# Performance work log

Measured on AMD Instinct MI355X. Metric: run time of the kernel, lower is better.

## Reference

```python
import jax, jax.numpy as jnp
import numpy as np

PAD, BOS, EOS, UNK = 0, 1, 2, 3
B, S, V, D, L = 256, 512, 50000, 256, 128

def setup_inputs() -> dict:
    key = jax.random.key(0)
    ks = jax.random.split(key, 12)
    vocab_tensor = jax.random.randint(ks[0], (B, S), 4, V)
    parent_idx = jax.random.randint(ks[1], (B, S), 0, S)
    pbond = jax.random.randint(ks[2], (B, S), 0, 4)
    bond = jax.random.randint(ks[3], (B, S), 0, 4)
    patom = jax.random.randint(ks[4], (B, S), 0, 16)
    atom = jax.random.randint(ks[5], (B, S), 0, 16)
    btype = jax.random.randint(ks[6], (B, S), 0, 4)
    order_tensor = jnp.stack([parent_idx, pbond, bond, patom, atom, btype], axis=-1)
    lengths = jax.random.randint(ks[7], (B,), 1, S + 1)
    mask_tensor = jnp.arange(S)[None, :] < lengths[:, None]  # ragged prefix masks
    eps = jax.random.normal(ks[8], (B, L), dtype=jnp.float32)
    sc = 1.0 / np.sqrt(D)
    emb = jax.random.normal(ks[9], (V, D), dtype=jnp.float32) * sc
    Wm = jax.random.normal(ks[10], (D, L), dtype=jnp.float32) * sc
    Wv = jax.random.normal(ks[11], (D, L), dtype=jnp.float32) * sc
    Wlin = jax.random.normal(jax.random.fold_in(key, 20), (L, D), dtype=jnp.float32) / np.sqrt(L)
    Wout = jax.random.normal(jax.random.fold_in(key, 21), (D, D), dtype=jnp.float32) * sc
    return {
        'vocab_tensor': vocab_tensor, 'order_tensor': order_tensor, 'mask_tensor': mask_tensor,
        'eps': eps, 'emb': emb, 'Wm': Wm, 'bm': jnp.zeros((L,), jnp.float32),
        'Wv': Wv, 'bv': jnp.zeros((L,), jnp.float32), 'Wlin': Wlin,
        'blin': jnp.zeros((D,), jnp.float32), 'Wout': Wout, 'bout': jnp.zeros((D,), jnp.float32),
    }

def _forward(vocab_tensor, order_tensor, mask_tensor, eps, emb, Wm, bm, Wv, bv, Wlin, blin, Wout, bout):
    # --- mask bond-pos columns (torch.where assignments, vectorized) ---
    # (columns 1 and 2 set to -1 where masked; kept implicitly via vt/pad handling)
    # --- calc_chem_z path: masked vocab, parent gather, edge one-hot ---
    vt = jnp.where(mask_tensor, vocab_tensor, PAD)                      # [B,S]
    vocab_emb = emb[vt]                                                 # [B,S,D]
    oi = order_tensor[..., 0]
    oi = jnp.where(oi == -1, BOS, oi)
    parent = jnp.where(mask_tensor, jnp.take_along_axis(vt, oi, axis=1), PAD)
    parent = parent.at[:, 0].set(BOS)
    parent_emb = emb[parent]                                            # [B,S,D]
    idx = jnp.clip(order_tensor[..., 5] - 1, -1, None)
    edge_type = jnp.where((idx >= 0)[..., None],
                          jax.nn.one_hot(jnp.clip(idx, 0), 3, dtype=jnp.float32), 0.0)  # [B,S,3]
    # pooling stand-in for (undefined) StructureEncoder -> [B,D]
    m = mask_tensor[..., None].astype(jnp.float32)
    enc = ((vocab_emb + parent_emb) * m).sum(1) / jnp.maximum(m.sum(1), 1.0)
    enc = enc * (1.0 + 0.0 * edge_type.sum())  # keep edge_type in graph
    # --- LatentSampler ---
    mean = enc @ Wm + bm
    log_var = enc @ Wv + bv
    z = mean + eps * jnp.exp(0.5 * log_var)
    memory = z @ Wlin + blin                                            # [B,D]
    # --- vectorized bos/eos/pad sequence assembly (the hot loop in torch) ---
    inp = jnp.concatenate([jnp.full((B, 1), BOS, vocab_tensor.dtype), vocab_tensor], axis=1)  # [B,S+1]
    mask_ex = jnp.concatenate([jnp.ones((B, 1), bool), mask_tensor], axis=1)
    tgt = jnp.roll(inp, -1, axis=1)
    first_false = jnp.argmax(~mask_ex, axis=1)                          # first eos position
    has_false = jnp.any(~mask_ex, axis=1)
    pos = jnp.arange(S + 1)[None, :]
    tgt = jnp.where(has_false[:, None] & (pos == first_false[:, None] - 1), EOS, tgt)
    kill = has_false[:, None] & (pos >= first_false[:, None])
    tgt = jnp.where(kill, PAD, tgt)
    inp = jnp.where(kill, PAD, inp)
    # edge_index assembly (faithful, consumed by decoder in original)
    padneg = jnp.full((B, 1), -1, order_tensor.dtype)
    edge_index = jnp.concatenate([padneg, jnp.where(mask_tensor, order_tensor[..., 0], -2) + 1], axis=1)
    # --- embedding lookups + decoder stand-in + output head ---
    node_embed = emb[inp]                                               # [B,S+1,D]
    dec = node_embed + memory[:, None, :]
    dec = dec + 0.0 * edge_index[..., None].astype(jnp.float32)         # keep edge_index in graph
    word_emb = dec @ Wout + bout
    tgt_emb = emb[tgt]
    valid = (tgt != PAD)
    sq = (word_emb - tgt_emb) ** 2 * valid[..., None]
    token_loss = sq.sum() / jnp.maximum(valid.sum() * D, 1).astype(jnp.float32)
    kl = -0.5 * jnp.sum(1.0 + log_var - mean ** 2 - jnp.exp(log_var)) / B
    return token_loss, kl

def reference(vocab_tensor, order_tensor, mask_tensor, eps, emb, Wm, bm, Wv, bv, Wlin, blin, Wout, bout):
    return _forward(vocab_tensor, order_tensor, mask_tensor, eps, emb, Wm, bm, Wv, bv, Wlin, blin, Wout, bout)
```

## Files before the change

### kernel.cpp

```cpp
#include <hip/hip_runtime.h>

#define B_ 256
#define S_ 512
#define V_ 50000
#define D_ 256
#define L_ 128
#define NGB 512
#define NENC 256
#define NCH (V_ / 16)
#define NSPLIT 8
#define K2B (B_ * NSPLIT)

typedef __attribute__((ext_vector_type(8))) short short8;
typedef __attribute__((ext_vector_type(4))) float floatx4;

#define OFF_SQP 16
#define OFF_KL  (OFF_SQP + K2B)
#define OFF_CNT (OFF_KL + 256)
#define OFF_Q   (OFF_CNT + 256)
#define OFF_P   (OFF_Q + B_ * D_)

__device__ __forceinline__ unsigned short f2bf(float x) {
    unsigned u = __float_as_uint(x);
    u += 0x7FFFu + ((u >> 16) & 1u);
    return (unsigned short)(u >> 16);
}
__device__ __forceinline__ float bf2f(unsigned short u) {
    return __uint_as_float(((unsigned)u) << 16);
}

__global__ __launch_bounds__(256, 2) void fused1(
    const int* __restrict__ vocab, const int* __restrict__ order,
    const int* __restrict__ mask, const float* __restrict__ emb,
    const float* __restrict__ eps, const float* __restrict__ Wm,
    const float* __restrict__ bm, const float* __restrict__ Wv,
    const float* __restrict__ bv, const float* __restrict__ Wlin,
    const float* __restrict__ blin, const float* __restrict__ Wout,
    const float* __restrict__ bout, float* __restrict__ ws) {
    __shared__ __align__(16) char smem[11904];
    const int tid = threadIdx.x;

    if (blockIdx.x < NGB) {
        unsigned short* __restrict__ P = (unsigned short*)(ws + OFF_P);
        const int lane = tid & 63, wv = tid >> 6;
        const int lo = lane & 15, hi = lane >> 4;
        short8 bfr[4][8];
#pragma unroll
        for (int nt = 0; nt < 4; ++nt)
#pragma unroll
            for (int kk = 0; kk < 8; ++kk) {
                const float* wp = Wout + (size_t)(hi * 8 + kk * 32) * D_ +
                                  wv * 64 + nt * 16 + lo;
                short8 w;
#pragma unroll
                for (int e = 0; e < 8; ++e) w[e] = (short)f2bf(wp[(size_t)e * D_]);
                bfr[nt][kk] = w;
            }
        int ch = blockIdx.x;
        float4 R[4];
        {
            const float4* src = (const float4*)emb + (size_t)ch * 1024;
#pragma unroll
            for (int i = 0; i < 4; ++i) R[i] = src[i * 256 + tid];
        }
        for (; ch < NCH; ch += NGB) {
#pragma unroll
            for (int i = 0; i < 4; ++i) {
                const int e = (i * 256 + tid) * 4;
                const int row = e >> 8, colb = (e & 255) * 2;
                const int byt = (row * 512 + colb) ^ ((row & 7) << 4);
                ushort4 h;
                h.x = f2bf(R[i].x); h.y = f2bf(R[i].y);
                h.z = f2bf(R[i].z); h.w = f2bf(R[i].w);
                *(ushort4*)(smem + byt) = h;
            }
            __syncthreads();
            const int chn = ch + NGB;
            float4 Rn[4] = {R[0], R[1], R[2], R[3]};
            if (chn < NCH) {
                const float4* src = (const float4*)emb + (size_t)chn * 1024;
#pragma unroll
                for (int i = 0; i < 4; ++i) Rn[i] = src[i * 256 + tid];
            }
            floatx4 acc[4];
#pragma unroll
            for (int nt = 0; nt < 4; ++nt) acc[nt] = (floatx4){0.f, 0.f, 0.f, 0.f};
#pragma unroll
            for (int kk = 0; kk < 8; ++kk) {
                const int byt = (lo * 512 + hi * 16 + kk * 64) ^ ((lo & 7) << 4);
                short8 a = *(const short8*)(smem + byt);
#pragma unroll
                for (int nt = 0; nt < 4; ++nt)
                    acc[nt] = __builtin_amdgcn_mfma_f32_16x16x32_bf16(
                        a, bfr[nt][kk], acc[nt], 0, 0, 0);
            }
#pragma unroll
            for (int r = 0; r < 4; ++r) {
                unsigned short* prow =
                    P + (size_t)(ch * 16 + hi * 4 + r) * D_ + wv * 64 + lo;
#pragma unroll
                for (int nt = 0; nt < 4; ++nt) prow[nt * 16] = f2bf(acc[nt][r]);
            }
            __syncthreads();
#pragma unroll
            for (int i = 0; i < 4; ++i) R[i] = Rn[i];
        }
        return;
    }
    int* s_id1 = (int*)smem;
    int* s_id2 = s_id1 + S_;
    float4* s_part = (float4*)(smem + 4096);
    float* s_enc = (float*)(smem + 7168);
    float* s_mean = (float*)(smem + 8192);
    float* s_lv = (float*)(smem + 8704);
    float* s_z = (float*)(smem + 9216);
    float* s_mem = (float*)(smem + 9728);
    float* s_red = (float*)(smem + 10752);
    int* s_cntp = (int*)(smem + 11776);
    const int b = blockIdx.x - NGB;
    if (tid == 0) *s_cntp = 0;
    __syncthreads();
    for (int j = tid; j < S_; j += 256) {
        const int mk = mask[b * S_ + j];
        int id1 = 0, id2 = 0;
        if (mk) {
            id1 = vocab[b * S_ + j];
            if (j == 0) {
                id2 = 1;
            } else {
                int oi = order[(size_t)(b * S_ + j) * 6];
                if (oi == -1) oi = 1;
                id2 = mask[b * S_ + oi] ? vocab[b * S_ + oi] : 0;
            }
        }
        s_id1[j] = id1;
        s_id2[j] = id2;
        unsigned long long bal = __ballot(mk != 0);
        if ((tid & 63) == 0) atomicAdd(s_cntp, __popcll(bal));
    }
    __syncthreads();
    const int cnt = *s_cntp;
    const int jg = tid >> 6, d4 = tid & 63;
    const float4* eb4 = (const float4*)emb;
    float4 a = {0.f, 0.f, 0.f, 0.f};
#pragma unroll 4
    for (int j = jg; j < cnt; j += 4) {
        float4 x = eb4[(size_t)s_id1[j] * 64 + d4];
        float4 y = eb4[(size_t)s_id2[j] * 64 + d4];
        a.x += x.x + y.x; a.y += x.y + y.y;
        a.z += x.z + y.z; a.w += x.w + y.w;
    }
    if (jg) s_part[(jg - 1) * 64 + d4] = a;
    __syncthreads();
    if (jg == 0) {
#pragma unroll
        for (int g = 0; g < 3; ++g) {
            float4 p = s_part[g * 64 + d4];
            a.x += p.x; a.y += p.y; a.z += p.z; a.w += p.w;
        }
        const float inv = 1.f / fmaxf((float)cnt, 1.f);
        a.x *= inv; a.y *= inv; a.z *= inv; a.w *= inv;
        ((float4*)s_enc)[d4] = a;
    }
    __syncthreads();
    {
        const int l = tid & (L_ - 1);
        const float* W = (tid < L_) ? Wm : Wv;
        const float* bb = (tid < L_) ? bm : bv;
        float dot = bb[l];
        for (int d = 0; d < D_; ++d) dot = fmaf(s_enc[d], W[d * L_ + l], dot);
        if (tid < L_) s_mean[l] = dot; else s_lv[l] = dot;
    }
    __syncthreads();
    float klp = 0.f;
    if (tid < L_) {
        float mn = s_mean[tid], lv = s_lv[tid];
        s_z[tid] = mn + eps[b * L_ + tid] * expf(0.5f * lv);
        klp = 1.f + lv - mn * mn - expf(lv);
    }
    s_red[tid] = klp;
    __syncthreads();
    for (int s = 128; s > 0; s >>= 1) {
        if (tid < s) s_red[tid] += s_red[tid + s];
        __syncthreads();
    }
    if (tid == 0) {
        ws[OFF_KL + b] = s_red[0];
        ((int*)ws)[OFF_CNT + b] = cnt;
    }
    {
        float mem = blin[tid];
        for (int l2 = 0; l2 < L_; ++l2) mem = fmaf(s_z[l2], Wlin[l2 * D_ + tid], mem);
        s_mem[tid] = mem;
    }
    __syncthreads();
    {
        float qv = bout[tid];
        for (int k = 0; k < D_; ++k) qv = fmaf(s_mem[k], Wout[k * D_ + tid], qv);
        ws[OFF_Q + b * D_ + tid] = qv;
    }
}

__global__ __launch_bounds__(256) void scan2(const int* __restrict__ vocab,
                                             const float* __restrict__ emb,
                                             float* __restrict__ ws) {
    __shared__ int s_sid[80];
    __shared__ float s_wred[4];
    const int tid = threadIdx.x;
    const int b = blockIdx.x >> 3, part = blockIdx.x & 7;
    const unsigned short* __restrict__ P = (const unsigned short*)(ws + OFF_P);
    const int cnt = ((const int*)ws)[OFF_CNT + b];
    const int npos = cnt + 1;
    const int per = (npos + NSPLIT - 1) / NSPLIT;
    const int j0 = part * per;
    const int jend = min(j0 + per, npos);
    const int lo_s = (j0 > 0) ? j0 - 1 : 0;
    const int nstage = min(jend, cnt) - lo_s;
    if (tid < nstage) s_sid[tid] = vocab[b * S_ + lo_s + tid];
    __syncthreads();
    const int jgq = tid >> 6, lane = tid & 63, c = lane * 4;
    const float4 q4 = *(const float4*)(ws + OFF_Q + b * D_ + c);
    float acc = 0.f;
    for (int jj = j0 + jgq * 4; jj < jend; jj += 16) {
        int inp[4], tgt[4];
        float wgt[4];
#pragma unroll
        for (int u = 0; u < 4; ++u) {
            const int j = jj + u;
            const bool v = (j < jend);
            const int jc = v ? j : jj;
            inp[u] = (jc == 0) ? 1 : s_sid[jc - 1 - lo_s];
            tgt[u] = (jc < cnt) ? s_sid[jc - lo_s] : ((cnt < S_) ? 2 : 1);
            wgt[u] = v ? 1.f : 0.f;
        }
        ushort4 pv[4];
        float4 tv[4];
#pragma unroll
        for (int u = 0; u < 4; ++u) {
            pv[u] = *(const ushort4*)(P + (size_t)inp[u] * D_ + c);
            tv[u] = *(const float4*)(emb + (size_t)tgt[u] * D_ + c);
        }
#pragma unroll
        for (int u = 0; u < 4; ++u) {
            float d0 = bf2f(pv[u].x) + q4.x - tv[u].x;
            float d1 = bf2f(pv[u].y) + q4.y - tv[u].y;
            float d2 = bf2f(pv[u].z) + q4.z - tv[u].z;
            float d3 = bf2f(pv[u].w) + q4.w - tv[u].w;
            float s = fmaf(d0, d0, fmaf(d1, d1, fmaf(d2, d2, d3 * d3)));
            acc = fmaf(wgt[u], s, acc);
        }
    }
#pragma unroll
    for (int off = 32; off; off >>= 1) acc += __shfl_down(acc, off, 64);
    if (lane == 0) s_wred[jgq] = acc;
    __syncthreads();
    if (tid == 0)
        ws[OFF_SQP + blockIdx.x] = s_wred[0] + s_wred[1] + s_wred[2] + s_wred[3];
}

__global__ __launch_bounds__(256) void finalize3(const float* __restrict__ ws,
                                                 float* __restrict__ out) {
    __shared__ float s_red[256];
    const int tid = threadIdx.x;
    float sq = 0.f;
#pragma unroll
    for (int i = 0; i < NSPLIT; ++i) sq += ws[OFF_SQP + i * 256 + tid];
    s_red[tid] = sq;
    __syncthreads();
    for (int s = 128; s > 0; s >>= 1) {
        if (tid < s) s_red[tid] += s_red[tid + s];
        __syncthreads();
    }
    const float sq_tot = s_red[0];
    __syncthreads();
    s_red[tid] = ws[OFF_KL + tid];
    __syncthreads();
    for (int s = 128; s > 0; s >>= 1) {
        if (tid < s) s_red[tid] += s_red[tid + s];
        __syncthreads();
    }
    const float kl_tot = s_red[0];
    __syncthreads();
    s_red[tid] = (float)(((const int*)ws)[OFF_CNT + tid] + 1);
    __syncthreads();
    for (int s = 128; s > 0; s >>= 1) {
        if (tid < s) s_red[tid] += s_red[tid + s];
        __syncthreads();
    }
    if (tid == 0) {
        float denom = s_red[0] * (float)D_;
        if (denom < 1.f) denom = 1.f;
        out[0] = sq_tot / denom;
        out[1] = -0.5f * kl_tot / (float)B_;
    }
}

extern "C" void kernel_launch(void* const* d_in, const int* in_sizes, int n_in,
                              void* d_out, int out_size, void* d_ws, size_t ws_size,
                              hipStream_t stream) {
    const int* vocab = (const int*)d_in[0];
    const int* order = (const int*)d_in[1];
    const int* mask  = (const int*)d_in[2];
    const float* eps  = (const float*)d_in[3];
    const float* emb  = (const float*)d_in[4];
    const float* Wm   = (const float*)d_in[5];
    const float* bm   = (const float*)d_in[6];
    const float* Wv   = (const float*)d_in[7];
    const float* bv   = (const float*)d_in[8];
    const float* Wlin = (const float*)d_in[9];
    const float* blin = (const float*)d_in[10];
    const float* Wout = (const float*)d_in[11];
    const float* bout = (const float*)d_in[12];

    float* ws = (float*)d_ws;
    fused1<<<NGB + NENC, 256, 0, stream>>>(vocab, order, mask, emb, eps, Wm, bm,
                                           Wv, bv, Wlin, blin, Wout, bout, ws);
    scan2<<<K2B, 256, 0, stream>>>(vocab, emb, ws);
    finalize3<<<1, 256, 0, stream>>>(ws, (float*)d_out);
}
```

Measured before the change: 172.0 us.

## Emit bf16 embedding copy and stage projected rows through LDS for coalesced stores

The fused projection kernel now writes a bf16 copy of each embedding chunk (already converted in shared memory) to a workspace buffer. Its projected output rows are staged through shared memory so they can be written with wide coalesced stores instead of scattered 2-byte stores. The scan kernel then gathers target embeddings as bf16 rather than fp32, halving the bytes of its random row reads. The cost is an extra bf16 table write per pass, a larger shared-memory footprint, and lower precision in the loss target term.

New measurement: 172.2 us. About the same (+0.1%).

```diff
diff --git a/kernel.cpp b/kernel.cpp
--- a/kernel.cpp
+++ b/kernel.cpp
@@ -19,6 +19,7 @@
 #define OFF_CNT (OFF_KL + 256)
 #define OFF_Q   (OFF_CNT + 256)
 #define OFF_P   (OFF_Q + B_ * D_)
+#define OFF_EB  (OFF_P + V_ * D_ / 2)
 
 __device__ __forceinline__ unsigned short f2bf(float x) {
     unsigned u = __float_as_uint(x);
@@ -37,11 +38,12 @@
     const float* __restrict__ bv, const float* __restrict__ Wlin,
     const float* __restrict__ blin, const float* __restrict__ Wout,
     const float* __restrict__ bout, float* __restrict__ ws) {
-    __shared__ __align__(16) char smem[11904];
+    __shared__ __align__(16) char smem[16384];
     const int tid = threadIdx.x;
 
     if (blockIdx.x < NGB) {
         unsigned short* __restrict__ P = (unsigned short*)(ws + OFF_P);
+        unsigned short* __restrict__ EB = (unsigned short*)(ws + OFF_EB);
         const int lane = tid & 63, wv = tid >> 6;
         const int lo = lane & 15, hi = lane >> 4;
         short8 bfr[4][8];
@@ -94,14 +96,32 @@
                     acc[nt] = __builtin_amdgcn_mfma_f32_16x16x32_bf16(
                         a, bfr[nt][kk], acc[nt], 0, 0, 0);
             }
+            {
+                const int o0 = tid * 32;
+                const int sw = ((o0 >> 9) & 7) << 4;
+                ushort4 e0 = *(const ushort4*)(smem + (o0 ^ sw));
+                ushort4 e1 = *(const ushort4*)(smem + ((o0 + 16) ^ sw));
+                ushort4* dst = (ushort4*)((char*)EB + (size_t)ch * 8192 + o0);
+                dst[0] = e0; dst[1] = e1;
+            }
 #pragma unroll
             for (int r = 0; r < 4; ++r) {
-                unsigned short* prow =
-                    P + (size_t)(ch * 16 + hi * 4 + r) * D_ + wv * 64 + lo;
-#pragma unroll
-                for (int nt = 0; nt < 4; ++nt) prow[nt * 16] = f2bf(acc[nt][r]);
+                const int row = hi * 4 + r;
+#pragma unroll
+                for (int nt = 0; nt < 4; ++nt) {
+                    const int col = wv * 64 + nt * 16 + lo;
+                    *(unsigned short*)(smem + 8192 + row * 512 + col * 2) =
+                        f2bf(acc[nt][r]);
+                }
             }
             __syncthreads();
+            {
+                const int o0 = tid * 32;
+                ushort4 c0 = *(const ushort4*)(smem + 8192 + o0);
+                ushort4 c1 = *(const ushort4*)(smem + 8192 + o0 + 16);
+                ushort4* dst = (ushort4*)((char*)P + (size_t)ch * 8192 + o0);
+                dst[0] = c0; dst[1] = c1;
+            }
 #pragma unroll
             for (int i = 0; i < 4; ++i) R[i] = Rn[i];
         }
@@ -202,13 +222,13 @@
 }
 
 __global__ __launch_bounds__(256) void scan2(const int* __restrict__ vocab,
-                                             const float* __restrict__ emb,
                                              float* __restrict__ ws) {
     __shared__ int s_sid[80];
     __shared__ float s_wred[4];
     const int tid = threadIdx.x;
     const int b = blockIdx.x >> 3, part = blockIdx.x & 7;
     const unsigned short* __restrict__ P = (const unsigned short*)(ws + OFF_P);
+    const unsigned short* __restrict__ EB = (const unsigned short*)(ws + OFF_EB);
     const int cnt = ((const int*)ws)[OFF_CNT + b];
     const int npos = cnt + 1;
     const int per = (npos + NSPLIT - 1) / NSPLIT;
@@ -233,19 +253,18 @@
             tgt[u] = (jc < cnt) ? s_sid[jc - lo_s] : ((cnt < S_) ? 2 : 1);
             wgt[u] = v ? 1.f : 0.f;
         }
-        ushort4 pv[4];
-        float4 tv[4];
+        ushort4 pv[4], tv[4];
 #pragma unroll
         for (int u = 0; u < 4; ++u) {
             pv[u] = *(const ushort4*)(P + (size_t)inp[u] * D_ + c);
-            tv[u] = *(const float4*)(emb + (size_t)tgt[u] * D_ + c);
+            tv[u] = *(const ushort4*)(EB + (size_t)tgt[u] * D_ + c);
         }
 #pragma unroll
         for (int u = 0; u < 4; ++u) {
-            float d0 = bf2f(pv[u].x) + q4.x - tv[u].x;
-            float d1 = bf2f(pv[u].y) + q4.y - tv[u].y;
-            float d2 = bf2f(pv[u].z) + q4.z - tv[u].z;
-            float d3 = bf2f(pv[u].w) + q4.w - tv[u].w;
+            float d0 = bf2f(pv[u].x) + q4.x - bf2f(tv[u].x);
+            float d1 = bf2f(pv[u].y) + q4.y - bf2f(tv[u].y);
+            float d2 = bf2f(pv[u].z) + q4.z - bf2f(tv[u].z);
+            float d3 = bf2f(pv[u].w) + q4.w - bf2f(tv[u].w);
             float s = fmaf(d0, d0, fmaf(d1, d1, fmaf(d2, d2, d3 * d3)));
             acc = fmaf(wgt[u], s, acc);
         }
@@ -315,6 +334,6 @@
     float* ws = (float*)d_ws;
     fused1<<<NGB + NENC, 256, 0, stream>>>(vocab, order, mask, emb, eps, Wm, bm,
                                            Wv, bv, Wlin, blin, Wout, bout, ws);
-    scan2<<<K2B, 256, 0, stream>>>(vocab, emb, ws);
+    scan2<<<K2B, 256, 0, stream>>>(vocab, ws);
     finalize3<<<1, 256, 0, stream>>>(ws, (float*)d_out);
 }
```
